# Optimization experiments

Hardware: AMD Instinct MI355X
Metric: run time of the kernel (lower is better)

## Reference

```python
import jax, jax.numpy as jnp
import numpy as np

B, N, DIM = 16, 2048, 256  # dim = 8 * win_length (win_length=32)


def setup_inputs() -> dict:
    key = jax.random.key(0)
    k_x, k_w, k_b = jax.random.split(key, 3)
    x = jax.random.normal(k_x, (B, N, DIM), dtype=jnp.float32)
    # nn.Linear(dim, dim): y = x @ W.T + b
    W_q = jax.random.normal(k_w, (DIM, DIM), dtype=jnp.float32) / np.sqrt(DIM)
    b_q = jax.random.normal(k_b, (DIM,), dtype=jnp.float32) * 0.01
    return {"input": x, "W_q": W_q, "b_q": b_q}


def reference(input, W_q, b_q):
    # Linear projection (dropout is identity in eval mode)
    p = jnp.einsum("bnd,ed->bne", input, W_q) + b_q  # [B, N, DIM]
    # Pairwise cosine similarity: normalize once, then one Gram matmul.
    # This is exactly dot(p_i, p_j) / (sqrt(dot(p_i,p_i)) * sqrt(dot(p_j,p_j)))
    # from the original nested-loop implementation.
    norm = jnp.sqrt(jnp.sum(p * p, axis=-1, keepdims=True))  # [B, N, 1]
    pn = p / norm
    attn_raw = jnp.einsum("bnd,bmd->bnm", pn, pn)  # [B, N, N], symmetric
    return attn_raw
```

## Files before the change

kernel.cpp:

```cpp
#include <hip/hip_runtime.h>
#include <hip/hip_bf16.h>


typedef __bf16 bf16x8 __attribute__((ext_vector_type(8)));
typedef float  f32x4  __attribute__((ext_vector_type(4)));

__device__ __forceinline__ void gl_lds16(const void* g, void* l) {
  __builtin_amdgcn_global_load_lds((const __attribute__((address_space(1))) void*)g,
                                   (__attribute__((address_space(3))) void*)l, 16, 0, 0);
}

__device__ __forceinline__ bf16x8 pack8(f32x4 a, f32x4 b) {
  bf16x8 r;
  r[0] = (__bf16)a[0]; r[1] = (__bf16)a[1]; r[2] = (__bf16)a[2]; r[3] = (__bf16)a[3];
  r[4] = (__bf16)b[0]; r[5] = (__bf16)b[1]; r[6] = (__bf16)b[2]; r[7] = (__bf16)b[3];
  return r;
}

__global__ __launch_bounds__(512, 1) void proj_kernel(
    const float* __restrict__ x, const float* __restrict__ W,
    const float* __restrict__ bq, __bf16* __restrict__ pn) {
  __shared__ __attribute__((aligned(16))) char ldsW[131072];
  const int t = threadIdx.x;
  const int lane = t & 63;
  const int w = t >> 6;

  #pragma unroll
  for (int it = 0; it < 16; ++it) {
    int base = (it * 512 + t) * 8;
    int row  = base >> 8;
    int colb = (base & 255) * 2;
    f32x4 v0 = *(const f32x4*)(W + base);
    f32x4 v1 = *(const f32x4*)(W + base + 4);
    *(bf16x8*)(ldsW + row * 512 + (colb ^ ((row & 7) << 4))) = pack8(v0, v1);
  }
  __syncthreads();

  const int r0 = blockIdx.x * 128 + w * 16;
  const int arow = r0 + (lane & 15);
  const float* xrow = x + (size_t)arow * 256 + (lane >> 4) * 8;
  bf16x8 afr[8];
  #pragma unroll
  for (int kk = 0; kk < 8; ++kk) {
    f32x4 v0 = *(const f32x4*)(xrow + kk * 32);
    f32x4 v1 = *(const f32x4*)(xrow + kk * 32 + 4);
    afr[kk] = pack8(v0, v1);
  }

  f32x4 acc[16];
  #pragma unroll
  for (int ct = 0; ct < 16; ++ct) acc[ct] = (f32x4){0.f, 0.f, 0.f, 0.f};
  const int kb0 = (lane >> 4) * 16;
  #pragma unroll
  for (int ct = 0; ct < 16; ++ct) {
    int brow = ct * 16 + (lane & 15);
    const char* wb = ldsW + brow * 512;
    int sw = (brow & 7) << 4;
    #pragma unroll
    for (int kk = 0; kk < 8; ++kk) {
      bf16x8 bf = *(const bf16x8*)(wb + ((kk * 64 + kb0) ^ sw));
      acc[ct] = __builtin_amdgcn_mfma_f32_16x16x32_bf16(afr[kk], bf, acc[ct], 0, 0, 0);
    }
  }

  float bc[16];
  #pragma unroll
  for (int ct = 0; ct < 16; ++ct) bc[ct] = bq[ct * 16 + (lane & 15)];
  #pragma unroll
  for (int ct = 0; ct < 16; ++ct) {
    #pragma unroll
    for (int r = 0; r < 4; ++r) acc[ct][r] += bc[ct];
  }
  #pragma unroll
  for (int r = 0; r < 4; ++r) {
    float s = 0.f;
    #pragma unroll
    for (int ct = 0; ct < 16; ++ct) s += acc[ct][r] * acc[ct][r];
    s += __shfl_xor(s, 1); s += __shfl_xor(s, 2);
    s += __shfl_xor(s, 4); s += __shfl_xor(s, 8);
    float rn = rsqrtf(s);
    int rowg = r0 + (lane >> 4) * 4 + r;
    __bf16* dst = pn + (size_t)rowg * 256 + (lane & 15);
    #pragma unroll
    for (int ct = 0; ct < 16; ++ct) dst[ct * 16] = (__bf16)(acc[ct][r] * rn);
  }
}

__global__ __launch_bounds__(512, 4) void gram_kernel(
    const __bf16* __restrict__ pn, float* __restrict__ out) {
  __shared__ __attribute__((aligned(16))) char lds[65536];
  const int t = threadIdx.x;
  const int lane = t & 63;
  const int w = t >> 6;
  const int wr = w >> 1;
  const int wc = w & 1;
  const int bid = blockIdx.x;
  const int batch = bid >> 5;
  const int stripe = (bid >> 1) & 15;
  const int jhalf = bid & 1;
  const char* pb = (const char*)(pn + (size_t)batch * 2048 * 256);
  const int i0 = stripe * 128;
  const int kb0 = (lane >> 4) * 16;

  #pragma unroll
  for (int i = 0; i < 8; ++i) {
    int off = (i * 512 + t) * 16;
    int row = off >> 9;
    int kb  = off & 511;
    gl_lds16(pb + (size_t)(i0 + row) * 512 + (kb ^ ((row & 7) << 4)),
             lds + i * 8192 + w * 1024);
  }
  __syncthreads();

  bf16x8 afr[2][8];
  #pragma unroll
  for (int fr = 0; fr < 2; ++fr) {
    int row = wr * 32 + fr * 16 + (lane & 15);
    const char* ab = lds + row * 512;
    int sw = (row & 7) << 4;
    #pragma unroll
    for (int kk = 0; kk < 8; ++kk)
      afr[fr][kk] = *(const bf16x8*)(ab + ((kk * 64 + kb0) ^ sw));
  }
  __syncthreads();

  const int jbase = jhalf * 1024;
  float* ob = out + (size_t)batch * 2048 * 2048;
  const int ro0 = i0 + wr * 32 + (lane >> 4) * 4;

  #pragma unroll
  for (int i = 0; i < 4; ++i) {
    int off = (i * 512 + t) * 16;
    int row = off >> 9;
    int kb  = off & 511;
    gl_lds16(pb + (size_t)(jbase + row) * 512 + (kb ^ ((row & 7) << 4)),
             lds + i * 8192 + w * 1024);
  }
  __syncthreads();

  for (int jj = 0; jj < 16; ++jj) {
    const char* buf = lds + (jj & 1) * 32768;
    if (jj < 15) {
      char* nb = lds + ((jj + 1) & 1) * 32768;
      int j0 = jbase + (jj + 1) * 64;
      #pragma unroll
      for (int i = 0; i < 4; ++i) {
        int off = (i * 512 + t) * 16;
        int row = off >> 9;
        int kb  = off & 511;
        gl_lds16(pb + (size_t)(j0 + row) * 512 + (kb ^ ((row & 7) << 4)),
                 nb + i * 8192 + w * 1024);
      }
    }
    f32x4 acc[2][2];
    #pragma unroll
    for (int m = 0; m < 2; ++m)
      #pragma unroll
      for (int n = 0; n < 2; ++n) acc[m][n] = (f32x4){0.f, 0.f, 0.f, 0.f};
    #pragma unroll
    for (int kk = 0; kk < 8; ++kk) {
      bf16x8 bfr[2];
      #pragma unroll
      for (int n = 0; n < 2; ++n) {
        int row = wc * 32 + n * 16 + (lane & 15);
        bfr[n] = *(const bf16x8*)(buf + row * 512 + ((kk * 64 + kb0) ^ ((row & 7) << 4)));
      }
      #pragma unroll
      for (int m = 0; m < 2; ++m)
        #pragma unroll
        for (int n = 0; n < 2; ++n)
          acc[m][n] = __builtin_amdgcn_mfma_f32_16x16x32_bf16(afr[m][kk], bfr[n], acc[m][n], 0, 0, 0);
    }
    __syncthreads();
    int co0 = jbase + jj * 64 + wc * 32 + (lane & 15);
    #pragma unroll
    for (int m = 0; m < 2; ++m)
      #pragma unroll
      for (int n = 0; n < 2; ++n)
        #pragma unroll
        for (int r = 0; r < 4; ++r)
          __builtin_nontemporal_store(acc[m][n][r],
              &ob[(size_t)(ro0 + m * 16 + r) * 2048 + (co0 + n * 16)]);
  }
}

extern "C" void kernel_launch(void* const* d_in, const int* in_sizes, int n_in,
                              void* d_out, int out_size, void* d_ws, size_t ws_size,
                              hipStream_t stream) {
  const float* x  = (const float*)d_in[0];
  const float* Wq = (const float*)d_in[1];
  const float* bq = (const float*)d_in[2];
  float* out = (float*)d_out;
  __bf16* pn = (__bf16*)d_ws;

  proj_kernel<<<dim3(256), dim3(512), 0, stream>>>(x, Wq, bq, pn);
  gram_kernel<<<dim3(512), dim3(512), 0, stream>>>(pn, out);
}
```

Before: 350.6 us.

## Remap gram block IDs, replace syncthreads with counted waits, use plain stores

The gram kernel remaps blockIdx so that consecutive hardware block IDs, which are distributed across XCDs, land on different batches and stripes. It also swaps the two __syncthreads per iteration for a single s_barrier at the top of the loop. An explicit s_waitcnt vmcnt(16) after the stores waits only for the prefetch loads to finish, so output stores can stay in flight across iterations. B-fragment row offsets and swizzles are hoisted out of the loop, and nontemporal stores become ordinary stores. The hand-counted vmcnt assumes a fixed number of outstanding memory operations, so a change in how the compiler emits stores could break correctness.

```diff
diff --git a/kernel.cpp b/kernel.cpp
--- a/kernel.cpp
+++ b/kernel.cpp
@@ -94,10 +94,10 @@
   const int w = t >> 6;
   const int wr = w >> 1;
   const int wc = w & 1;
-  const int bid = blockIdx.x;
-  const int batch = bid >> 5;
-  const int stripe = (bid >> 1) & 15;
-  const int jhalf = bid & 1;
+  const int vb = (blockIdx.x & 7) * 64 + (blockIdx.x >> 3);
+  const int batch = vb >> 5;
+  const int stripe = (vb >> 1) & 15;
+  const int jhalf = vb & 1;
   const char* pb = (const char*)(pn + (size_t)batch * 2048 * 256);
   const int i0 = stripe * 128;
   const int kb0 = (lane >> 4) * 16;
@@ -127,6 +127,10 @@
   const int jbase = jhalf * 1024;
   float* ob = out + (size_t)batch * 2048 * 2048;
   const int ro0 = i0 + wr * 32 + (lane >> 4) * 4;
+  const int brow0 = wc * 32 + (lane & 15);
+  const int brow1 = brow0 + 16;
+  const int bsw0 = (brow0 & 7) << 4;
+  const int bsw1 = (brow1 & 7) << 4;
 
   #pragma unroll
   for (int i = 0; i < 4; ++i) {
@@ -136,10 +140,10 @@
     gl_lds16(pb + (size_t)(jbase + row) * 512 + (kb ^ ((row & 7) << 4)),
              lds + i * 8192 + w * 1024);
   }
-  __syncthreads();
+  asm volatile("s_waitcnt vmcnt(0)" ::: "memory");
 
   for (int jj = 0; jj < 16; ++jj) {
-    const char* buf = lds + (jj & 1) * 32768;
+    __builtin_amdgcn_s_barrier();
     if (jj < 15) {
       char* nb = lds + ((jj + 1) & 1) * 32768;
       int j0 = jbase + (jj + 1) * 64;
@@ -152,6 +156,9 @@
                  nb + i * 8192 + w * 1024);
       }
     }
+    asm volatile("" ::: "memory");
+
+    const char* buf = lds + (jj & 1) * 32768;
     f32x4 acc[2][2];
     #pragma unroll
     for (int m = 0; m < 2; ++m)
@@ -159,19 +166,17 @@
       for (int n = 0; n < 2; ++n) acc[m][n] = (f32x4){0.f, 0.f, 0.f, 0.f};
     #pragma unroll
     for (int kk = 0; kk < 8; ++kk) {
+      int kb = kk * 64 + kb0;
       bf16x8 bfr[2];
-      #pragma unroll
-      for (int n = 0; n < 2; ++n) {
-        int row = wc * 32 + n * 16 + (lane & 15);
-        bfr[n] = *(const bf16x8*)(buf + row * 512 + ((kk * 64 + kb0) ^ ((row & 7) << 4)));
-      }
+      bfr[0] = *(const bf16x8*)(buf + brow0 * 512 + (kb ^ bsw0));
+      bfr[1] = *(const bf16x8*)(buf + brow1 * 512 + (kb ^ bsw1));
       #pragma unroll
       for (int m = 0; m < 2; ++m)
         #pragma unroll
         for (int n = 0; n < 2; ++n)
           acc[m][n] = __builtin_amdgcn_mfma_f32_16x16x32_bf16(afr[m][kk], bfr[n], acc[m][n], 0, 0, 0);
     }
-    __syncthreads();
+
     int co0 = jbase + jj * 64 + wc * 32 + (lane & 15);
     #pragma unroll
     for (int m = 0; m < 2; ++m)
@@ -179,8 +184,10 @@
       for (int n = 0; n < 2; ++n)
         #pragma unroll
         for (int r = 0; r < 4; ++r)
-          __builtin_nontemporal_store(acc[m][n][r],
-              &ob[(size_t)(ro0 + m * 16 + r) * 2048 + (co0 + n * 16)]);
+          ob[(size_t)(ro0 + m * 16 + r) * 2048 + (co0 + n * 16)] = acc[m][n][r];
+
+    if (jj < 15)
+      asm volatile("s_waitcnt vmcnt(16)" ::: "memory");
   }
 }
 
```

After: 322.9 us. 7.9% less time.
